# Performance work log

Hardware: AMD Instinct MI355X
Metric: run time of the kernel (lower is better)

The kernel has to match this reference:

```python
import jax, jax.numpy as jnp
import numpy as np

EPS = np.float32(np.finfo(float).eps)  # 2.220446049250313e-16, matches torch code
TOP_K = 2


def setup_inputs() -> dict:
    key = jax.random.key(0)
    ks = jax.random.split(key, 7)
    B, D, H, E = 8192, 1024, 4096, 8
    # init scales mirror the torch MLP init (std = sqrt(2/(m+n)), sqrt(1/m))
    return {
        "inp": jax.random.normal(ks[0], (B, D), dtype=jnp.float32),
        "gate_w": jax.random.normal(ks[1], (E, D), dtype=jnp.float32) * np.sqrt(1.0 / D).astype(np.float32),
        "gate_b": jax.random.normal(ks[2], (E,), dtype=jnp.float32) * 0.01,
        "W1": jax.random.normal(ks[3], (E, H, D), dtype=jnp.float32) * np.sqrt(2.0 / (H + D)).astype(np.float32),
        "b1": jax.random.normal(ks[4], (E, H), dtype=jnp.float32) * np.sqrt(1.0 / H).astype(np.float32),
        "W2": jax.random.normal(ks[5], (E, D, H), dtype=jnp.float32) * np.sqrt(2.0 / (D + H)).astype(np.float32),
        "b2": jax.random.normal(ks[6], (E, D), dtype=jnp.float32) * np.sqrt(1.0 / D).astype(np.float32),
    }


def _moe_forward(inp, gate_w, gate_b, W1, b1, W2, b2):
    B = inp.shape[0]
    E = gate_w.shape[0]
    # --- NaiveGate: linear -> top-k -> softmax -> scatter into dense gates ---
    logits = inp @ gate_w.T + gate_b                      # [B, E]
    top_vals, top_idx = jax.lax.top_k(logits, TOP_K)      # [B, k]
    top_gates = jax.nn.softmax(top_vals, axis=-1)         # top_k > 1 branch
    gates = jnp.zeros((B, E), dtype=jnp.float32)
    gates = gates.at[jnp.arange(B)[:, None], top_idx].set(top_gates)

    # --- Experts: 2-layer MLP, ReLU after every linear (sigmoid_layer=-1) ---
    h = jax.nn.relu(jnp.einsum('bd,ehd->ebh', inp, W1) + b1[:, None, :])   # [E, B, H]
    out = jax.nn.relu(jnp.einsum('ebh,edh->ebd', h, W2) + b2[:, None, :])  # [E, B, D]

    # --- SparseDispatcher.combine: exp -> gate-weighted scatter-sum -> +eps -> log ---
    # Dense-equivalent: gates are exactly zero for non-routed (token, expert)
    # pairs, so the weighted sum matches the sparse scatter exactly.
    combined = jnp.einsum('be,ebd->bd', gates, jnp.exp(out))
    return jnp.log(combined + EPS)


def reference(inp, gate_w, gate_b, W1, b1, W2, b2):
    return _moe_forward(inp, gate_w, gate_b, W1, b1, W2, b2)
```

## Files before the change

### kernel.cpp

```cpp
#include <hip/hip_runtime.h>
#include <hip/hip_bf16.h>
#include <math.h>

#define B_TOK 8192
#define DDIM  1024
#define HDIM  4096
#define NEXP  8
#define CAP   17408

typedef unsigned short u16;
using f32x4  = __attribute__((ext_vector_type(4))) float;
using bf16x8 = __attribute__((ext_vector_type(8))) short;

__device__ __forceinline__ u16 f2bf(float f) {
  union { float f; unsigned u; } v; v.f = f;
  unsigned r = v.u + 0x7FFFu + ((v.u >> 16) & 1u);
  return (u16)(r >> 16);
}

__device__ __forceinline__ void load_lds16(const void* g, void* l) {
  __builtin_amdgcn_global_load_lds((const __attribute__((address_space(1))) void*)g,
                                   (__attribute__((address_space(3))) void*)l,
                                   16, 0, 0);
}

__global__ __launch_bounds__(256) void cvtw_kernel(const float4* __restrict__ w1,
                                                   const float4* __restrict__ w2,
                                                   ushort4* __restrict__ w1b,
                                                   ushort4* __restrict__ w2b, int n4each) {
  for (int i = blockIdx.x * 256 + threadIdx.x; i < 2 * n4each; i += gridDim.x * 256) {
    const float4* src = (i < n4each) ? w1 : w2;
    ushort4*      dst = (i < n4each) ? w1b : w2b;
    int j = (i < n4each) ? i : i - n4each;
    float4 v = src[j];
    ushort4 o;
    o.x = f2bf(v.x); o.y = f2bf(v.y); o.z = f2bf(v.z); o.w = f2bf(v.w);
    dst[j] = o;
  }
}

__global__ __launch_bounds__(256) void gate_kernel(
    const float* __restrict__ inp, const float* __restrict__ gw,
    const float* __restrict__ gb, int* __restrict__ tok_e,
    float* __restrict__ tok_g, int* __restrict__ counts,
    ushort4* __restrict__ Xb4)
{
  int gtid = blockIdx.x * 256 + threadIdx.x;
  int tok  = gtid >> 6;
  int lane = threadIdx.x & 63;
  if (tok >= B_TOK) return;
  const float4* X = (const float4*)(inp + (size_t)tok * DDIM);
  float4 x[4];
#pragma unroll
  for (int j = 0; j < 4; ++j) x[j] = X[j * 64 + lane];
  ushort4* Xrow = Xb4 + (size_t)tok * (DDIM / 4);
#pragma unroll
  for (int j = 0; j < 4; ++j) {
    ushort4 o;
    o.x = f2bf(x[j].x); o.y = f2bf(x[j].y); o.z = f2bf(x[j].z); o.w = f2bf(x[j].w);
    Xrow[j * 64 + lane] = o;
  }
  float lg[NEXP];
#pragma unroll
  for (int e = 0; e < NEXP; ++e) {
    const float4* W = (const float4*)(gw + e * DDIM);
    double s = 0.0;
#pragma unroll
    for (int j = 0; j < 4; ++j) {
      float4 w = W[j * 64 + lane];
      s += (double)x[j].x * w.x + (double)x[j].y * w.y
         + (double)x[j].z * w.z + (double)x[j].w * w.w;
    }
#pragma unroll
    for (int o = 32; o > 0; o >>= 1) s += __shfl_xor(s, o);
    lg[e] = (float)(s + (double)gb[e]);
  }
  if (lane == 0) {
    int i0 = 0; float v0 = lg[0];
#pragma unroll
    for (int e = 1; e < NEXP; ++e) if (lg[e] > v0) { v0 = lg[e]; i0 = e; }
    int i1 = -1; float v1 = -3.4e38f;
#pragma unroll
    for (int e = 0; e < NEXP; ++e) if (e != i0 && lg[e] > v1) { v1 = lg[e]; i1 = e; }
    float t   = __expf(v1 - v0);
    float inv = 1.0f / (1.0f + t);
    tok_e[2 * tok] = i0; tok_e[2 * tok + 1] = i1;
    tok_g[2 * tok] = inv; tok_g[2 * tok + 1] = t * inv;
    atomicAdd(&counts[i0], 1);
    atomicAdd(&counts[i1], 1);
  }
}

__global__ __launch_bounds__(256) void scatter_kernel(
    const int* __restrict__ tok_e, const float* __restrict__ tok_g,
    const int* __restrict__ counts, int* __restrict__ cursors,
    int* __restrict__ slot_token, float* __restrict__ slot_gate,
    int* __restrict__ tok_slot,
    int* __restrict__ offs, int* __restrict__ padded)
{
  __shared__ int soffs[NEXP];
  if (threadIdx.x == 0) {
    int off = 0;
    for (int e = 0; e < NEXP; ++e) {
      soffs[e] = off;
      int p = (counts[e] + 127) & ~127;
      off += p;
      if (blockIdx.x == 0) { offs[e] = soffs[e]; padded[e] = p; }
    }
  }
  __syncthreads();
  int b = blockIdx.x * 256 + threadIdx.x;
  if (b >= B_TOK) return;
#pragma unroll
  for (int k = 0; k < 2; ++k) {
    int e   = tok_e[2 * b + k];
    float g = tok_g[2 * b + k];
    int pos = atomicAdd(&cursors[e], 1);
    int s   = soffs[e] + pos;
    slot_token[s] = b;
    slot_gate[s]  = g;
    tok_slot[2 * b + k] = s;
  }
}


#define STAGE(kt_) do {                                                   \
    _Pragma("unroll") for (int g = 0; g < 4; ++g) {                       \
      load_lds16(pAg[g] + (kt_) * 64, &As[(g * 256 + tid) * 8]);           \
      load_lds16(pBg[g] + (kt_) * 64, &Bs[(g * 256 + tid) * 8]);           \
    } } while (0)

#define GEMM_BODY(NT_) do {                                               \
    const int NT = (NT_);                                                 \
    _Pragma("unroll 1")                                                   \
    for (int t = 0; t < NT; ++t) {                                        \
      STAGE(t);                                                           \
      __syncthreads();                                                    \
      bf16x8 af[4][2], bfr[4][2];                                         \
      _Pragma("unroll") for (int m = 0; m < 4; ++m)                       \
        _Pragma("unroll") for (int kk = 0; kk < 2; ++kk)                  \
          af[m][kk] = *(const bf16x8*)&As[(wm + m*16 + fr)*64             \
                                        + (((kk*4 + fq) ^ fr7) * 8)];     \
      _Pragma("unroll") for (int n = 0; n < 4; ++n)                       \
        _Pragma("unroll") for (int kk = 0; kk < 2; ++kk)                  \
          bfr[n][kk] = *(const bf16x8*)&Bs[(wn + n*16 + fr)*64            \
                                        + (((kk*4 + fq) ^ fr7) * 8)];     \
      _Pragma("unroll") for (int kk = 0; kk < 2; ++kk)                    \
      _Pragma("unroll") for (int m = 0; m < 4; ++m)                       \
      _Pragma("unroll") for (int n = 0; n < 4; ++n)                       \
        acc[m][n] = __builtin_amdgcn_mfma_f32_16x16x32_bf16(              \
            af[m][kk], bfr[n][kk], acc[m][n], 0, 0, 0);                   \
      __syncthreads();                                                    \
    } } while (0)

__global__ __launch_bounds__(256, 4) void gemm1_kernel(
    const u16* __restrict__ Xb, const u16* __restrict__ W1b,
    const float* __restrict__ b1, const int* __restrict__ slot_token,
    const int* __restrict__ offs, const int* __restrict__ padded,
    u16* __restrict__ Hb)
{
  const int h   = blockIdx.x + 32 * (blockIdx.y + 64 * blockIdx.z);
  const int e   = h & 7;
  const int r   = h >> 3;
  const int mi  = r >> 5;
  const int nti = r & 31;
  if (mi * 128 >= padded[e]) return;
  const int base_slot = offs[e] + mi * 128;
  const int n0 = nti * 128;

  __shared__ __align__(16) u16 As[8192];
  __shared__ __align__(16) u16 Bs[8192];
  __shared__ int toks[128];

  const int tid = threadIdx.x;
  if (tid < 128) toks[tid] = slot_token[base_slot + tid];
  __syncthreads();

  const u16* pAg[4];
  const u16* pBg[4];
#pragma unroll
  for (int g = 0; g < 4; ++g) {
    int i = g * 256 + tid, rr = i >> 3, sl = i & 7;
    int kc = (sl ^ (rr & 7)) * 8;
    pAg[g] = Xb + (size_t)toks[rr] * DDIM + kc;
    pBg[g] = W1b + ((size_t)e * HDIM + (size_t)(n0 + rr)) * DDIM + kc;
  }

  const int wave = tid >> 6, lane = tid & 63;
  const int wm = (wave >> 1) * 64, wn = (wave & 1) * 64;
  const int fr = lane & 15, fq = lane >> 4, fr7 = fr & 7;

  f32x4 acc[4][4];
#pragma unroll
  for (int m = 0; m < 4; ++m)
#pragma unroll
    for (int n = 0; n < 4; ++n) acc[m][n] = f32x4{0.f, 0.f, 0.f, 0.f};

  GEMM_BODY(DDIM / 64);

#pragma unroll
  for (int n = 0; n < 4; ++n) {
    int col = n0 + wn + n * 16 + fr;
    float bias = b1[e * HDIM + col];
#pragma unroll
    for (int m = 0; m < 4; ++m) {
      int row0 = wm + m * 16 + fq * 4;
#pragma unroll
      for (int j = 0; j < 4; ++j) {
        float v = acc[m][n][j] + bias;
        v = v > 0.f ? v : 0.f;
        Hb[(size_t)(base_slot + row0 + j) * HDIM + col] = f2bf(v);
      }
    }
  }
}

__global__ __launch_bounds__(256, 4) void gemm2_kernel(
    const u16* __restrict__ Hb, const u16* __restrict__ W2b,
    const float* __restrict__ b2, const float* __restrict__ slot_gate,
    const int* __restrict__ offs, const int* __restrict__ padded,
    float* __restrict__ P)
{
  const int h   = blockIdx.x + 8 * (blockIdx.y + 64 * blockIdx.z);
  const int e   = h & 7;
  const int r   = h >> 3;
  const int mi  = r >> 3;
  const int nti = r & 7;
  if (mi * 128 >= padded[e]) return;
  const int base_slot = offs[e] + mi * 128;
  const int n0 = nti * 128;

  __shared__ __align__(16) u16 As[8192];
  __shared__ __align__(16) u16 Bs[8192];
  __shared__ float gts[128];

  const int tid = threadIdx.x;
  if (tid < 128) gts[tid] = slot_gate[base_slot + tid];
  __syncthreads();

  const u16* pAg[4];
  const u16* pBg[4];
#pragma unroll
  for (int g = 0; g < 4; ++g) {
    int i = g * 256 + tid, rr = i >> 3, sl = i & 7;
    int kc = (sl ^ (rr & 7)) * 8;
    pAg[g] = Hb + (size_t)(base_slot + rr) * HDIM + kc;
    pBg[g] = W2b + ((size_t)e * DDIM + (size_t)(n0 + rr)) * HDIM + kc;
  }

  const int wave = tid >> 6, lane = tid & 63;
  const int wm = (wave >> 1) * 64, wn = (wave & 1) * 64;
  const int fr = lane & 15, fq = lane >> 4, fr7 = fr & 7;

  f32x4 acc[4][4];
#pragma unroll
  for (int m = 0; m < 4; ++m)
#pragma unroll
    for (int n = 0; n < 4; ++n) acc[m][n] = f32x4{0.f, 0.f, 0.f, 0.f};

  GEMM_BODY(HDIM / 64);

#pragma unroll
  for (int n = 0; n < 4; ++n) {
    int col = n0 + wn + n * 16 + fr;
    float bias = b2[e * DDIM + col];
#pragma unroll
    for (int m = 0; m < 4; ++m) {
      int row0 = wm + m * 16 + fq * 4;
#pragma unroll
      for (int j = 0; j < 4; ++j) {
        int row = row0 + j;
        float v = acc[m][n][j] + bias;
        v = v > 0.f ? v : 0.f;
        P[(size_t)(base_slot + row) * DDIM + col] = gts[row] * __expf(v);
      }
    }
  }
}

__global__ __launch_bounds__(256) void combine_kernel(
    const float4* __restrict__ P4, const int* __restrict__ tok_slot,
    float4* __restrict__ out4)
{
  const float EPS = 2.220446049250313e-16f;
  const int total = B_TOK * (DDIM / 4);
  for (int i = blockIdx.x * 256 + threadIdx.x; i < total; i += gridDim.x * 256) {
    int tok = i >> 8, d4 = i & 255;
    int s0 = tok_slot[2 * tok], s1 = tok_slot[2 * tok + 1];
    float4 a = P4[(size_t)s0 * (DDIM / 4) + d4];
    float4 b = P4[(size_t)s1 * (DDIM / 4) + d4];
    float4 v;
    v.x = logf(a.x + b.x + EPS);
    v.y = logf(a.y + b.y + EPS);
    v.z = logf(a.z + b.z + EPS);
    v.w = logf(a.w + b.w + EPS);
    out4[i] = v;
  }
}

extern "C" void kernel_launch(void* const* d_in, const int* in_sizes, int n_in,
                              void* d_out, int out_size, void* d_ws, size_t ws_size,
                              hipStream_t stream)
{
  const float* inp = (const float*)d_in[0];
  const float* gw  = (const float*)d_in[1];
  const float* gb  = (const float*)d_in[2];
  const float* W1  = (const float*)d_in[3];
  const float* b1  = (const float*)d_in[4];
  const float* W2  = (const float*)d_in[5];
  const float* b2  = (const float*)d_in[6];
  float* out = (float*)d_out;

  char* ws = (char*)d_ws;
  size_t off = 0;
  auto alloc = [&](size_t bytes) {
    void* p = ws + off;
    off = (off + bytes + 255) & ~(size_t)255;
    return p;
  };
  u16*   Xb  = (u16*)alloc((size_t)B_TOK * DDIM * 2);
  u16*   W1b = (u16*)alloc((size_t)NEXP * HDIM * DDIM * 2);
  float* P   = (float*)Xb;
  u16*   W2b = (u16*)alloc((size_t)NEXP * DDIM * HDIM * 2);
  u16*   Hb  = (u16*)alloc((size_t)CAP * HDIM * 2);
  int*   slot_token = (int*)alloc(CAP * 4);
  float* slot_gate  = (float*)alloc(CAP * 4);
  int*   tok_e    = (int*)alloc(B_TOK * 2 * 4);
  float* tok_g    = (float*)alloc(B_TOK * 2 * 4);
  int*   tok_slot = (int*)alloc(B_TOK * 2 * 4);
  int*   counts  = (int*)alloc(32);
  int*   cursors = (int*)alloc(32);
  int*   offs    = (int*)alloc(32);
  int*   padded  = (int*)alloc(32);

  (void)hipMemsetAsync(counts, 0, 288, stream);
  (void)hipMemsetAsync(slot_token, 0, (size_t)CAP * 8, stream);

  gate_kernel<<<B_TOK / 4, 256, 0, stream>>>(inp, gw, gb, tok_e, tok_g, counts,
                                             (ushort4*)Xb);
  cvtw_kernel<<<4096, 256, 0, stream>>>((const float4*)W1, (const float4*)W2,
                                        (ushort4*)W1b, (ushort4*)W2b,
                                        NEXP * HDIM * DDIM / 4);
  scatter_kernel<<<B_TOK / 256, 256, 0, stream>>>(tok_e, tok_g, counts, cursors,
                                                  slot_token, slot_gate, tok_slot,
                                                  offs, padded);

  gemm1_kernel<<<dim3(32, 64, NEXP), 256, 0, stream>>>(
      Xb, W1b, b1, slot_token, offs, padded, Hb);
  gemm2_kernel<<<dim3(8, 64, NEXP), 256, 0, stream>>>(
      Hb, W2b, b2, slot_gate, offs, padded, P);

  combine_kernel<<<2048, 256, 0, stream>>>((const float4*)P, tok_slot, (float4*)out);
}
```

Measured before the change: 723.5 us.

## Fuse fp32-to-bf16 weight conversion into GEMM B-tile loads

Removes the standalone weight conversion kernel and has both expert GEMMs load fp32 weight tiles into registers, convert to bf16, and write them to LDS, prefetching the next tile while the current one computes. This avoids a full pass over both weight tensors and the bf16 weight buffers. In exchange each GEMM reads twice as many weight bytes per tile, repeated across token tiles, and uses more registers, which may reduce occupancy.

Result: slower. 1.353 ms (+87.0%).

```diff
diff --git a/kernel.cpp b/kernel.cpp
--- a/kernel.cpp
+++ b/kernel.cpp
@@ -11,6 +11,7 @@
 typedef unsigned short u16;
 using f32x4  = __attribute__((ext_vector_type(4))) float;
 using bf16x8 = __attribute__((ext_vector_type(8))) short;
+using u16x8  = __attribute__((ext_vector_type(8))) unsigned short;
 
 __device__ __forceinline__ u16 f2bf(float f) {
   union { float f; unsigned u; } v; v.f = f;
@@ -22,21 +23,6 @@
   __builtin_amdgcn_global_load_lds((const __attribute__((address_space(1))) void*)g,
                                    (__attribute__((address_space(3))) void*)l,
                                    16, 0, 0);
-}
-
-__global__ __launch_bounds__(256) void cvtw_kernel(const float4* __restrict__ w1,
-                                                   const float4* __restrict__ w2,
-                                                   ushort4* __restrict__ w1b,
-                                                   ushort4* __restrict__ w2b, int n4each) {
-  for (int i = blockIdx.x * 256 + threadIdx.x; i < 2 * n4each; i += gridDim.x * 256) {
-    const float4* src = (i < n4each) ? w1 : w2;
-    ushort4*      dst = (i < n4each) ? w1b : w2b;
-    int j = (i < n4each) ? i : i - n4each;
-    float4 v = src[j];
-    ushort4 o;
-    o.x = f2bf(v.x); o.y = f2bf(v.y); o.z = f2bf(v.z); o.w = f2bf(v.w);
-    dst[j] = o;
-  }
 }
 
 __global__ __launch_bounds__(256) void gate_kernel(
@@ -124,17 +110,35 @@
 }
 
 
-#define STAGE(kt_) do {                                                   \
+#define STAGE_A(kt_) do {                                                 \
+    _Pragma("unroll") for (int g = 0; g < 4; ++g)                         \
+      load_lds16(pAg[g] + (kt_) * 64, &As[(g * 256 + tid) * 8]);           \
+  } while (0)
+
+#define LOADB(kt_) do {                                                   \
     _Pragma("unroll") for (int g = 0; g < 4; ++g) {                       \
-      load_lds16(pAg[g] + (kt_) * 64, &As[(g * 256 + tid) * 8]);           \
-      load_lds16(pBg[g] + (kt_) * 64, &Bs[(g * 256 + tid) * 8]);           \
+      bnx[g][0] = *(const f32x4*)(pBf[g] + (size_t)(kt_) * 64);           \
+      bnx[g][1] = *(const f32x4*)(pBf[g] + (size_t)(kt_) * 64 + 4);       \
+    } } while (0)
+
+#define WRITEB do {                                                       \
+    _Pragma("unroll") for (int g = 0; g < 4; ++g) {                       \
+      u16x8 o;                                                            \
+      o[0] = f2bf(bnx[g][0][0]); o[1] = f2bf(bnx[g][0][1]);               \
+      o[2] = f2bf(bnx[g][0][2]); o[3] = f2bf(bnx[g][0][3]);               \
+      o[4] = f2bf(bnx[g][1][0]); o[5] = f2bf(bnx[g][1][1]);               \
+      o[6] = f2bf(bnx[g][1][2]); o[7] = f2bf(bnx[g][1][3]);               \
+      *(u16x8*)&Bs[(g * 256 + tid) * 8] = o;                              \
     } } while (0)
 
 #define GEMM_BODY(NT_) do {                                               \
     const int NT = (NT_);                                                 \
+    LOADB(0);                                                             \
     _Pragma("unroll 1")                                                   \
     for (int t = 0; t < NT; ++t) {                                        \
-      STAGE(t);                                                           \
+      STAGE_A(t);                                                         \
+      WRITEB;                                                             \
+      if (t + 1 < NT) LOADB(t + 1);                                       \
       __syncthreads();                                                    \
       bf16x8 af[4][2], bfr[4][2];                                         \
       _Pragma("unroll") for (int m = 0; m < 4; ++m)                       \
@@ -154,7 +158,7 @@
     } } while (0)
 
 __global__ __launch_bounds__(256, 4) void gemm1_kernel(
-    const u16* __restrict__ Xb, const u16* __restrict__ W1b,
+    const u16* __restrict__ Xb, const float* __restrict__ W1,
     const float* __restrict__ b1, const int* __restrict__ slot_token,
     const int* __restrict__ offs, const int* __restrict__ padded,
     u16* __restrict__ Hb)
@@ -176,14 +180,14 @@
   if (tid < 128) toks[tid] = slot_token[base_slot + tid];
   __syncthreads();
 
-  const u16* pAg[4];
-  const u16* pBg[4];
+  const u16*   pAg[4];
+  const float* pBf[4];
 #pragma unroll
   for (int g = 0; g < 4; ++g) {
     int i = g * 256 + tid, rr = i >> 3, sl = i & 7;
     int kc = (sl ^ (rr & 7)) * 8;
     pAg[g] = Xb + (size_t)toks[rr] * DDIM + kc;
-    pBg[g] = W1b + ((size_t)e * HDIM + (size_t)(n0 + rr)) * DDIM + kc;
+    pBf[g] = W1 + ((size_t)e * HDIM + (size_t)(n0 + rr)) * DDIM + kc;
   }
 
   const int wave = tid >> 6, lane = tid & 63;
@@ -195,6 +199,7 @@
   for (int m = 0; m < 4; ++m)
 #pragma unroll
     for (int n = 0; n < 4; ++n) acc[m][n] = f32x4{0.f, 0.f, 0.f, 0.f};
+  f32x4 bnx[4][2];
 
   GEMM_BODY(DDIM / 64);
 
@@ -216,7 +221,7 @@
 }
 
 __global__ __launch_bounds__(256, 4) void gemm2_kernel(
-    const u16* __restrict__ Hb, const u16* __restrict__ W2b,
+    const u16* __restrict__ Hb, const float* __restrict__ W2,
     const float* __restrict__ b2, const float* __restrict__ slot_gate,
     const int* __restrict__ offs, const int* __restrict__ padded,
     float* __restrict__ P)
@@ -238,14 +243,14 @@
   if (tid < 128) gts[tid] = slot_gate[base_slot + tid];
   __syncthreads();
 
-  const u16* pAg[4];
-  const u16* pBg[4];
+  const u16*   pAg[4];
+  const float* pBf[4];
 #pragma unroll
   for (int g = 0; g < 4; ++g) {
     int i = g * 256 + tid, rr = i >> 3, sl = i & 7;
     int kc = (sl ^ (rr & 7)) * 8;
     pAg[g] = Hb + (size_t)(base_slot + rr) * HDIM + kc;
-    pBg[g] = W2b + ((size_t)e * DDIM + (size_t)(n0 + rr)) * HDIM + kc;
+    pBf[g] = W2 + ((size_t)e * DDIM + (size_t)(n0 + rr)) * HDIM + kc;
   }
 
   const int wave = tid >> 6, lane = tid & 63;
@@ -257,6 +262,7 @@
   for (int m = 0; m < 4; ++m)
 #pragma unroll
     for (int n = 0; n < 4; ++n) acc[m][n] = f32x4{0.f, 0.f, 0.f, 0.f};
+  f32x4 bnx[4][2];
 
   GEMM_BODY(HDIM / 64);
 
@@ -319,10 +325,8 @@
     return p;
   };
   u16*   Xb  = (u16*)alloc((size_t)B_TOK * DDIM * 2);
-  u16*   W1b = (u16*)alloc((size_t)NEXP * HDIM * DDIM * 2);
-  float* P   = (float*)Xb;
-  u16*   W2b = (u16*)alloc((size_t)NEXP * DDIM * HDIM * 2);
   u16*   Hb  = (u16*)alloc((size_t)CAP * HDIM * 2);
+  float* P   = (float*)alloc((size_t)CAP * DDIM * 4);
   int*   slot_token = (int*)alloc(CAP * 4);
   float* slot_gate  = (float*)alloc(CAP * 4);
   int*   tok_e    = (int*)alloc(B_TOK * 2 * 4);
@@ -338,17 +342,14 @@
 
   gate_kernel<<<B_TOK / 4, 256, 0, stream>>>(inp, gw, gb, tok_e, tok_g, counts,
                                              (ushort4*)Xb);
-  cvtw_kernel<<<4096, 256, 0, stream>>>((const float4*)W1, (const float4*)W2,
-                                        (ushort4*)W1b, (ushort4*)W2b,
-                                        NEXP * HDIM * DDIM / 4);
   scatter_kernel<<<B_TOK / 256, 256, 0, stream>>>(tok_e, tok_g, counts, cursors,
                                                   slot_token, slot_gate, tok_slot,
                                                   offs, padded);
 
   gemm1_kernel<<<dim3(32, 64, NEXP), 256, 0, stream>>>(
-      Xb, W1b, b1, slot_token, offs, padded, Hb);
+      Xb, W1, b1, slot_token, offs, padded, Hb);
   gemm2_kernel<<<dim3(8, 64, NEXP), 256, 0, stream>>>(
-      Hb, W2b, b2, slot_gate, offs, padded, P);
+      Hb, W2, b2, slot_gate, offs, padded, P);
 
   combine_kernel<<<2048, 256, 0, stream>>>((const float4*)P, tok_slot, (float4*)out);
 }
```
